# Kernel optimization log

Measured on AMD Instinct MI355X. Metric: run time of the kernel, lower is better.

Reference implementation:

```python
import jax, jax.numpy as jnp
import numpy as np

EPS = 1e-7

def _cell(x_t, h, s_l, s_B, lambda_log, B):
    # x_t: [b, d], h/s_l: [b, n], s_B: [b, n, d], lambda_log: [n], B: [n, d]
    lam = jnp.exp(-jnp.exp(lambda_log))                    # [n]
    gamma = jnp.sqrt(1.0 - lam * lam + EPS)                # [n]
    Bx = x_t @ B.T                                         # [b, n]
    h1 = lam * h + gamma * Bx
    dlam = -lam * jnp.exp(lambda_log)                      # d lambda / d lambda_log
    s_l1 = h * dlam + lam * s_l + Bx * (-lam / gamma) * dlam
    s_B1 = lam[None, :, None] * s_B + gamma[None, :, None] * x_t[:, None, :]
    return h1, s_l1, s_B1

def setup_inputs() -> dict:
    key = jax.random.key(0)
    k1, k2, k3, k4 = jax.random.split(key, 4)
    S, BT, D, N, O = 256, 32, 128, 128, 128
    x = jax.random.normal(k1, (S, BT, D), dtype=jnp.float32)
    # torch init: lambda_log = log(-0.5*log(u1)) with rmin=0, rmax=1
    u1 = jax.random.uniform(k2, (N,), dtype=jnp.float32, minval=0.01, maxval=0.99)
    lambda_log = jnp.log(-0.5 * jnp.log(u1))
    B = jax.random.normal(k3, (N, D), dtype=jnp.float32) / np.sqrt(D)
    C = jax.random.normal(k4, (O, N), dtype=jnp.float32) / np.sqrt(N)
    return {"x": x, "lambda_log": lambda_log, "B": B, "C": C}

def reference(x, lambda_log, B, C):
    S, BT, D = x.shape
    N = B.shape[0]
    h0 = jnp.zeros((BT, N), x.dtype)
    sl0 = jnp.zeros((BT, N), x.dtype)
    sB0 = jnp.zeros((BT, N, D), x.dtype)

    def scan_fn(carry, x_t):
        h, s_l, s_B = carry
        h1, s_l1, s_B1 = _cell(x_t, h, s_l, s_B, lambda_log, B)
        return (h1, s_l1, s_B1), h1

    (hT, _, _), hs = jax.lax.scan(scan_fn, (h0, sl0, sB0), x)
    outputs = jnp.einsum('sbn,on->sbo', hs, C)  # h_t @ C^T per step
    return outputs, hT
```

## Files before the change

kernel.cpp:

```cpp
#include <hip/hip_runtime.h>

#define S_DIM 256
#define BT_DIM 32
#define D_DIM 128
#define N_DIM 128
#define O_DIM 128
#define SB (S_DIM * BT_DIM)
#define EPS 1e-7f

typedef short s16x8 __attribute__((ext_vector_type(8)));
typedef float fx4   __attribute__((ext_vector_type(4)));

union U8 { unsigned short u[8]; s16x8 v; };

__device__ __forceinline__ unsigned short f2bf(float f) {
    unsigned u = __builtin_bit_cast(unsigned, f);
    return (unsigned short)((u + 0x7fffu + ((u >> 16) & 1u)) >> 16);
}
__device__ __forceinline__ float bf2f(unsigned short h) {
    unsigned u = ((unsigned)h) << 16;
    return __builtin_bit_cast(float, u);
}
__device__ __forceinline__ void cvt8(const float4 f0, const float4 f1, s16x8& hi, s16x8& lo) {
    float f[8] = {f0.x, f0.y, f0.z, f0.w, f1.x, f1.y, f1.z, f1.w};
    U8 h, l;
    #pragma unroll
    for (int i = 0; i < 8; ++i) {
        unsigned short hb = f2bf(f[i]);
        h.u[i] = hb;
        l.u[i] = f2bf(f[i] - bf2f(hb));
    }
    hi = h.v; lo = l.v;
}
__device__ __forceinline__ void pack4(const float4 f, unsigned* hi2, unsigned* lo2) {
    float f_[4] = {f.x, f.y, f.z, f.w};
    unsigned short hb[4], lb[4];
    #pragma unroll
    for (int i = 0; i < 4; ++i) {
        hb[i] = f2bf(f_[i]);
        lb[i] = f2bf(f_[i] - bf2f(hb[i]));
    }
    hi2[0] = (unsigned)hb[0] | ((unsigned)hb[1] << 16);
    hi2[1] = (unsigned)hb[2] | ((unsigned)hb[3] << 16);
    lo2[0] = (unsigned)lb[0] | ((unsigned)lb[1] << 16);
    lo2[1] = (unsigned)lb[2] | ((unsigned)lb[3] << 16);
}

__global__ __launch_bounds__(256) void k1_gemm_scan(const float* __restrict__ X,
                                                    const float* __restrict__ lamlog,
                                                    const float* __restrict__ Bm,
                                                    unsigned short* __restrict__ hs_hi,
                                                    unsigned short* __restrict__ hs_lo,
                                                    float* __restrict__ hT) {
    __shared__ unsigned short Bhi[16][136];
    __shared__ unsigned short Blo[16][136];
    __shared__ float Bxs[S_DIM][17];
    __shared__ float carr[16][17];

    const int t  = threadIdx.x;
    const int b  = blockIdx.x >> 3;
    const int n0 = (blockIdx.x & 7) * 16;

    #pragma unroll
    for (int q = 0; q < 2; ++q) {
        const int id4 = t + 256 * q;
        const int row = id4 >> 5, c4 = id4 & 31;
        const float4 f = *reinterpret_cast<const float4*>(Bm + (size_t)(n0 + row) * D_DIM + c4 * 4);
        unsigned hi2[2], lo2[2];
        pack4(f, hi2, lo2);
        *reinterpret_cast<uint2*>(&Bhi[row][c4 * 4]) = make_uint2(hi2[0], hi2[1]);
        *reinterpret_cast<uint2*>(&Blo[row][c4 * 4]) = make_uint2(lo2[0], lo2[1]);
    }
    __syncthreads();

    const int w  = t >> 6, l = t & 63;
    const int lr = l & 15;
    const int lk = (l >> 4) * 8;

    s16x8 bh[4], bl[4];
    #pragma unroll
    for (int sl = 0; sl < 4; ++sl) {
        bh[sl] = *reinterpret_cast<const s16x8*>(&Bhi[lr][sl * 32 + lk]);
        bl[sl] = *reinterpret_cast<const s16x8*>(&Blo[lr][sl * 32 + lk]);
    }

    const float* __restrict__ xb = X + (size_t)b * D_DIM;
    #pragma unroll
    for (int q = 0; q < 4; ++q) {
        const int s0 = (w * 4 + q) * 16;
        const float* __restrict__ xr = xb + (size_t)(s0 + lr) * (BT_DIM * D_DIM);
        s16x8 ah[4], al[4];
        #pragma unroll
        for (int sl = 0; sl < 4; ++sl) {
            const float4 f0 = *reinterpret_cast<const float4*>(xr + sl * 32 + lk);
            const float4 f1 = *reinterpret_cast<const float4*>(xr + sl * 32 + lk + 4);
            cvt8(f0, f1, ah[sl], al[sl]);
        }
        fx4 acc = {0.f, 0.f, 0.f, 0.f};
        #pragma unroll
        for (int sl = 0; sl < 4; ++sl) {
            acc = __builtin_amdgcn_mfma_f32_16x16x32_bf16(ah[sl], bh[sl], acc, 0, 0, 0);
            acc = __builtin_amdgcn_mfma_f32_16x16x32_bf16(ah[sl], bl[sl], acc, 0, 0, 0);
            acc = __builtin_amdgcn_mfma_f32_16x16x32_bf16(al[sl], bh[sl], acc, 0, 0, 0);
        }
        #pragma unroll
        for (int r = 0; r < 4; ++r)
            Bxs[s0 + (l >> 4) * 4 + r][lr] = acc[r];
    }
    __syncthreads();

    const int j = t & 15;
    const int c = t >> 4;
    const float ll    = lamlog[n0 + j];
    const float lam   = expf(-expf(ll));
    const float gamma = sqrtf(1.f - lam * lam + EPS);
    const float l2 = lam * lam, l4 = l2 * l2, l8 = l4 * l4;
    const float lam16 = l8 * l8;

    float h = 0.f;
    #pragma unroll
    for (int i = 0; i < 16; ++i)
        h = fmaf(lam, h, gamma * Bxs[c * 16 + i][j]);
    carr[c][j] = h;
    __syncthreads();

    float Hb = 0.f;
    for (int cp = 0; cp < c; ++cp)
        Hb = fmaf(lam16, Hb, carr[cp][j]);

    h = Hb;
    #pragma unroll
    for (int i = 0; i < 16; ++i) {
        h = fmaf(lam, h, gamma * Bxs[c * 16 + i][j]);
        const size_t rg = (size_t)(c * 16 + i) * BT_DIM + b;
        const unsigned short hb = f2bf(h);
        hs_hi[rg * N_DIM + n0 + j] = hb;
        hs_lo[rg * N_DIM + n0 + j] = f2bf(h - bf2f(hb));
    }
    if (c == 15) hT[b * N_DIM + n0 + j] = h;
}

__global__ __launch_bounds__(256) void k2_outgemm(const unsigned short* __restrict__ hs_hi,
                                                  const unsigned short* __restrict__ hs_lo,
                                                  const float* __restrict__ Cm,
                                                  float* __restrict__ out) {
    __shared__ unsigned short Chi[128][136];
    __shared__ unsigned short Clo[128][136];

    const int t  = threadIdx.x;
    const int r0 = blockIdx.x * 32;

    #pragma unroll
    for (int q = 0; q < 16; ++q) {
        const int id4 = t + 256 * q;
        const int row = id4 >> 5, c4 = id4 & 31;
        const float4 f = *reinterpret_cast<const float4*>(Cm + (size_t)row * N_DIM + c4 * 4);
        unsigned hi2[2], lo2[2];
        pack4(f, hi2, lo2);
        *reinterpret_cast<uint2*>(&Chi[row][c4 * 4]) = make_uint2(hi2[0], hi2[1]);
        *reinterpret_cast<uint2*>(&Clo[row][c4 * 4]) = make_uint2(lo2[0], lo2[1]);
    }
    __syncthreads();

    const int w  = t >> 6, l = t & 63;
    const int lr = l & 15;
    const int lk = (l >> 4) * 8;
    const int rbase = r0 + 16 * (w & 1) + lr;

    s16x8 ah[4], al[4];
    #pragma unroll
    for (int sl = 0; sl < 4; ++sl) {
        ah[sl] = *reinterpret_cast<const s16x8*>(&hs_hi[(size_t)rbase * N_DIM + sl * 32 + lk]);
        al[sl] = *reinterpret_cast<const s16x8*>(&hs_lo[(size_t)rbase * N_DIM + sl * 32 + lk]);
    }

    #pragma unroll
    for (int q = 0; q < 4; ++q) {
        const int o0 = (w >> 1) * 64 + q * 16;
        fx4 acc = {0.f, 0.f, 0.f, 0.f};
        #pragma unroll
        for (int sl = 0; sl < 4; ++sl) {
            const s16x8 bh = *reinterpret_cast<const s16x8*>(&Chi[o0 + lr][sl * 32 + lk]);
            const s16x8 bl = *reinterpret_cast<const s16x8*>(&Clo[o0 + lr][sl * 32 + lk]);
            acc = __builtin_amdgcn_mfma_f32_16x16x32_bf16(ah[sl], bh, acc, 0, 0, 0);
            acc = __builtin_amdgcn_mfma_f32_16x16x32_bf16(ah[sl], bl, acc, 0, 0, 0);
            acc = __builtin_amdgcn_mfma_f32_16x16x32_bf16(al[sl], bh, acc, 0, 0, 0);
        }
        const int rw = r0 + 16 * (w & 1) + (l >> 4) * 4;
        #pragma unroll
        for (int r = 0; r < 4; ++r)
            out[(size_t)(rw + r) * O_DIM + o0 + lr] = acc[r];
    }
}

extern "C" void kernel_launch(void* const* d_in, const int* in_sizes, int n_in,
                              void* d_out, int out_size, void* d_ws, size_t ws_size,
                              hipStream_t stream) {
    const float* x          = (const float*)d_in[0];
    const float* lambda_log = (const float*)d_in[1];
    const float* B          = (const float*)d_in[2];
    const float* C          = (const float*)d_in[3];

    float* out = (float*)d_out;
    float* hT  = out + (size_t)SB * O_DIM;

    unsigned short* hs_hi = (unsigned short*)d_ws;
    unsigned short* hs_lo = hs_hi + (size_t)SB * N_DIM;

    k1_gemm_scan<<<256, 256, 0, stream>>>(x, lambda_log, B, hs_hi, hs_lo, hT);
    k2_outgemm<<<256, 256, 0, stream>>>(hs_hi, hs_lo, C, out);
}
```

Before: 75.29 us.

## Drop activation low-bf16 split and precompute C bf16 planes in extra blocks

Drops the low bf16 part of x and of the stored hidden states, cutting each split-precision product from three MFMAs to two and no longer writing or reading the hs_lo buffer. The bf16 hi/lo conversion of C moves out of every k2 block into eight extra blocks of k1, which write the planes to workspace. k2 then reads C fragments straight from global memory instead of staging them in LDS. This removes redundant conversion work, LDS traffic and a quarter of the MFMAs, at the cost of lower accuracy in both GEMMs, since activations now carry only bf16 precision.

Result: no change. 73.91 us (-1.8%).

```diff
diff --git a/kernel.cpp b/kernel.cpp
--- a/kernel.cpp
+++ b/kernel.cpp
@@ -21,16 +21,12 @@
     unsigned u = ((unsigned)h) << 16;
     return __builtin_bit_cast(float, u);
 }
-__device__ __forceinline__ void cvt8(const float4 f0, const float4 f1, s16x8& hi, s16x8& lo) {
+__device__ __forceinline__ s16x8 cvt8hi(const float4 f0, const float4 f1) {
     float f[8] = {f0.x, f0.y, f0.z, f0.w, f1.x, f1.y, f1.z, f1.w};
-    U8 h, l;
-    #pragma unroll
-    for (int i = 0; i < 8; ++i) {
-        unsigned short hb = f2bf(f[i]);
-        h.u[i] = hb;
-        l.u[i] = f2bf(f[i] - bf2f(hb));
-    }
-    hi = h.v; lo = l.v;
+    U8 h;
+    #pragma unroll
+    for (int i = 0; i < 8; ++i) h.u[i] = f2bf(f[i]);
+    return h.v;
 }
 __device__ __forceinline__ void pack4(const float4 f, unsigned* hi2, unsigned* lo2) {
     float f_[4] = {f.x, f.y, f.z, f.w};
@@ -49,15 +45,30 @@
 __global__ __launch_bounds__(256) void k1_gemm_scan(const float* __restrict__ X,
                                                     const float* __restrict__ lamlog,
                                                     const float* __restrict__ Bm,
+                                                    const float* __restrict__ Cm,
                                                     unsigned short* __restrict__ hs_hi,
-                                                    unsigned short* __restrict__ hs_lo,
+                                                    unsigned short* __restrict__ Chi,
+                                                    unsigned short* __restrict__ Clo,
                                                     float* __restrict__ hT) {
+    const int t = threadIdx.x;
+
+    if (blockIdx.x >= 256) {
+        const int id = (blockIdx.x - 256) * 256 + t;
+        const float4 f0 = reinterpret_cast<const float4*>(Cm)[id * 2];
+        const float4 f1 = reinterpret_cast<const float4*>(Cm)[id * 2 + 1];
+        unsigned h0[2], l0[2], h1[2], l1[2];
+        pack4(f0, h0, l0);
+        pack4(f1, h1, l1);
+        *reinterpret_cast<uint4*>(Chi + (size_t)id * 8) = make_uint4(h0[0], h0[1], h1[0], h1[1]);
+        *reinterpret_cast<uint4*>(Clo + (size_t)id * 8) = make_uint4(l0[0], l0[1], l1[0], l1[1]);
+        return;
+    }
+
     __shared__ unsigned short Bhi[16][136];
     __shared__ unsigned short Blo[16][136];
     __shared__ float Bxs[S_DIM][17];
     __shared__ float carr[16][17];
 
-    const int t  = threadIdx.x;
     const int b  = blockIdx.x >> 3;
     const int n0 = (blockIdx.x & 7) * 16;
 
@@ -89,19 +100,18 @@
     for (int q = 0; q < 4; ++q) {
         const int s0 = (w * 4 + q) * 16;
         const float* __restrict__ xr = xb + (size_t)(s0 + lr) * (BT_DIM * D_DIM);
-        s16x8 ah[4], al[4];
+        s16x8 ah[4];
         #pragma unroll
         for (int sl = 0; sl < 4; ++sl) {
             const float4 f0 = *reinterpret_cast<const float4*>(xr + sl * 32 + lk);
             const float4 f1 = *reinterpret_cast<const float4*>(xr + sl * 32 + lk + 4);
-            cvt8(f0, f1, ah[sl], al[sl]);
+            ah[sl] = cvt8hi(f0, f1);
         }
         fx4 acc = {0.f, 0.f, 0.f, 0.f};
         #pragma unroll
         for (int sl = 0; sl < 4; ++sl) {
             acc = __builtin_amdgcn_mfma_f32_16x16x32_bf16(ah[sl], bh[sl], acc, 0, 0, 0);
             acc = __builtin_amdgcn_mfma_f32_16x16x32_bf16(ah[sl], bl[sl], acc, 0, 0, 0);
-            acc = __builtin_amdgcn_mfma_f32_16x16x32_bf16(al[sl], bh[sl], acc, 0, 0, 0);
         }
         #pragma unroll
         for (int r = 0; r < 4; ++r)
@@ -133,46 +143,26 @@
     for (int i = 0; i < 16; ++i) {
         h = fmaf(lam, h, gamma * Bxs[c * 16 + i][j]);
         const size_t rg = (size_t)(c * 16 + i) * BT_DIM + b;
-        const unsigned short hb = f2bf(h);
-        hs_hi[rg * N_DIM + n0 + j] = hb;
-        hs_lo[rg * N_DIM + n0 + j] = f2bf(h - bf2f(hb));
+        hs_hi[rg * N_DIM + n0 + j] = f2bf(h);
     }
     if (c == 15) hT[b * N_DIM + n0 + j] = h;
 }
 
 __global__ __launch_bounds__(256) void k2_outgemm(const unsigned short* __restrict__ hs_hi,
-                                                  const unsigned short* __restrict__ hs_lo,
-                                                  const float* __restrict__ Cm,
+                                                  const unsigned short* __restrict__ Chi,
+                                                  const unsigned short* __restrict__ Clo,
                                                   float* __restrict__ out) {
-    __shared__ unsigned short Chi[128][136];
-    __shared__ unsigned short Clo[128][136];
-
     const int t  = threadIdx.x;
     const int r0 = blockIdx.x * 32;
-
-    #pragma unroll
-    for (int q = 0; q < 16; ++q) {
-        const int id4 = t + 256 * q;
-        const int row = id4 >> 5, c4 = id4 & 31;
-        const float4 f = *reinterpret_cast<const float4*>(Cm + (size_t)row * N_DIM + c4 * 4);
-        unsigned hi2[2], lo2[2];
-        pack4(f, hi2, lo2);
-        *reinterpret_cast<uint2*>(&Chi[row][c4 * 4]) = make_uint2(hi2[0], hi2[1]);
-        *reinterpret_cast<uint2*>(&Clo[row][c4 * 4]) = make_uint2(lo2[0], lo2[1]);
-    }
-    __syncthreads();
-
     const int w  = t >> 6, l = t & 63;
     const int lr = l & 15;
     const int lk = (l >> 4) * 8;
     const int rbase = r0 + 16 * (w & 1) + lr;
 
-    s16x8 ah[4], al[4];
-    #pragma unroll
-    for (int sl = 0; sl < 4; ++sl) {
+    s16x8 ah[4];
+    #pragma unroll
+    for (int sl = 0; sl < 4; ++sl)
         ah[sl] = *reinterpret_cast<const s16x8*>(&hs_hi[(size_t)rbase * N_DIM + sl * 32 + lk]);
-        al[sl] = *reinterpret_cast<const s16x8*>(&hs_lo[(size_t)rbase * N_DIM + sl * 32 + lk]);
-    }
 
     #pragma unroll
     for (int q = 0; q < 4; ++q) {
@@ -180,11 +170,10 @@
         fx4 acc = {0.f, 0.f, 0.f, 0.f};
         #pragma unroll
         for (int sl = 0; sl < 4; ++sl) {
-            const s16x8 bh = *reinterpret_cast<const s16x8*>(&Chi[o0 + lr][sl * 32 + lk]);
-            const s16x8 bl = *reinterpret_cast<const s16x8*>(&Clo[o0 + lr][sl * 32 + lk]);
+            const s16x8 bh = *reinterpret_cast<const s16x8*>(&Chi[(size_t)(o0 + lr) * N_DIM + sl * 32 + lk]);
+            const s16x8 bl = *reinterpret_cast<const s16x8*>(&Clo[(size_t)(o0 + lr) * N_DIM + sl * 32 + lk]);
             acc = __builtin_amdgcn_mfma_f32_16x16x32_bf16(ah[sl], bh, acc, 0, 0, 0);
             acc = __builtin_amdgcn_mfma_f32_16x16x32_bf16(ah[sl], bl, acc, 0, 0, 0);
-            acc = __builtin_amdgcn_mfma_f32_16x16x32_bf16(al[sl], bh, acc, 0, 0, 0);
         }
         const int rw = r0 + 16 * (w & 1) + (l >> 4) * 4;
         #pragma unroll
@@ -205,8 +194,9 @@
     float* hT  = out + (size_t)SB * O_DIM;
 
     unsigned short* hs_hi = (unsigned short*)d_ws;
-    unsigned short* hs_lo = hs_hi + (size_t)SB * N_DIM;
-
-    k1_gemm_scan<<<256, 256, 0, stream>>>(x, lambda_log, B, hs_hi, hs_lo, hT);
-    k2_outgemm<<<256, 256, 0, stream>>>(hs_hi, hs_lo, C, out);
-}
+    unsigned short* Chi   = hs_hi + (size_t)SB * N_DIM;
+    unsigned short* Clo   = Chi + O_DIM * N_DIM;
+
+    k1_gemm_scan<<<264, 256, 0, stream>>>(x, lambda_log, B, C, hs_hi, Chi, Clo, hT);
+    k2_outgemm<<<256, 256, 0, stream>>>(hs_hi, Chi, Clo, out);
+}
```
